# Optimization experiments

Measured on AMD Instinct MI355X. Metric: run time of the kernel, lower is better.

## Reference

```python
import jax, jax.numpy as jnp
import numpy as np

COMMIT_WEIGHT = 0.25


def setup_inputs() -> dict:
    key = jax.random.key(0)
    k1, k2 = jax.random.split(key)
    B, D, T, K = 8, 512, 2048, 8192
    x = jax.random.normal(k1, (B, D, T), dtype=jnp.float32)
    codebook = jax.random.normal(k2, (K, D), dtype=jnp.float32)
    return {"x": x, "codebook": codebook}


def reference(x, codebook):
    # x: [B, D, T] channels-first; VQ operates on [B, T, D]
    xt = jnp.transpose(x, (0, 2, 1))  # [B, T, D]
    x2 = jnp.sum(xt * xt, axis=-1, keepdims=True)          # [B, T, 1]
    e2 = jnp.sum(codebook * codebook, axis=-1)             # [K]
    xe = jnp.einsum('btd,kd->btk', xt, codebook)           # [B, T, K] (dominant GEMM)
    dists = x2 - 2.0 * xe + e2                             # [B, T, K]
    indices = jnp.argmin(dists, axis=-1)                   # [B, T] int
    quantized = codebook[indices]                          # [B, T, D] gather
    # commitment loss: ||sg(q) - x||^2 mean
    commit_loss = COMMIT_WEIGHT * jnp.mean(
        (jax.lax.stop_gradient(quantized) - xt) ** 2)
    # straight-through estimator
    quantized = xt + jax.lax.stop_gradient(quantized - xt)
    quantized = jnp.transpose(quantized, (0, 2, 1))        # back to [B, D, T]
    return quantized, indices, commit_loss
```

## Files before the change

kernel.cpp:

```cpp
#include <hip/hip_runtime.h>
#include <cstdint>
#include <cstddef>

#define B_   8
#define D_   512
#define T_   2048
#define K_   8192
#define BT_  (B_ * T_)
#define NQ_  ((size_t)B_ * D_ * T_)

typedef _Float16 f16x8 __attribute__((ext_vector_type(8)));
typedef _Float16 f16x4 __attribute__((ext_vector_type(4)));
typedef float    f32x4 __attribute__((ext_vector_type(4)));
typedef unsigned long long u64;
typedef unsigned int u32;

#define WS_SLOTS_OFF    0
#define WS_FIDX_OFF     393216
#define WS_PART_OFF     458752
#define WS_E2_OFF       460800
#define WS_XH_OFF       524288
#define WS_XL_OFF       (WS_XH_OFF + 16777216)
#define WS_CH_OFF       (WS_XL_OFF + 16777216)
#define WS_NEEDED       ((size_t)WS_CH_OFF + 8388608)

__device__ __forceinline__ void gload_lds16(const void* g, void* l) {
    __builtin_amdgcn_global_load_lds(
        (const __attribute__((address_space(1))) void*)g,
        (__attribute__((address_space(3))) void*)l, 16, 0, 0);
}

__device__ __forceinline__ u32 fkey(float f) {
    u32 u = __float_as_uint(f);
    u ^= (u32)((int)u >> 31) | 0x80000000u;
    return u;
}
__device__ __forceinline__ u64 umin64(u64 a, u64 b) { return a < b ? a : b; }
__device__ __forceinline__ u64 umax64(u64 a, u64 b) { return a > b ? a : b; }

__global__ __launch_bounds__(256) void k_e2(const float* __restrict__ cb,
                                            float* __restrict__ e2) {
    int k = blockIdx.x * 256 + threadIdx.x;
    const float4* row = (const float4*)(cb + (size_t)k * D_);
    float s = 0.f;
#pragma unroll 4
    for (int i = 0; i < D_ / 4; ++i) {
        float4 v = row[i];
        s = fmaf(v.x, v.x, s); s = fmaf(v.y, v.y, s);
        s = fmaf(v.z, v.z, s); s = fmaf(v.w, v.w, s);
    }
    e2[k] = s;
}

__global__ __launch_bounds__(256) void k_splitcb(const float* __restrict__ cb,
                                                 _Float16* __restrict__ ch) {
    size_t i = ((size_t)blockIdx.x * 256 + threadIdx.x) * 4;
    float4 v = *(const float4*)(cb + i);
    f16x4 h;
    h[0] = (_Float16)v.x; h[1] = (_Float16)v.y;
    h[2] = (_Float16)v.z; h[3] = (_Float16)v.w;
    *(f16x4*)(ch + i) = h;
}

__global__ __launch_bounds__(256) void k_splitx(const float* __restrict__ x,
                                                _Float16* __restrict__ xh,
                                                _Float16* __restrict__ xl) {
    int b  = blockIdx.z;
    int d0 = blockIdx.y * 64;
    int t0 = blockIdx.x * 64;
    int dl = threadIdx.x & 63;
    int tq = threadIdx.x >> 6;
    const float* px = x + ((size_t)b * D_ + (d0 + dl)) * T_ + t0;
#pragma unroll 4
    for (int i = 0; i < 16; ++i) {
        int t = tq * 16 + i;
        float v = px[t];
        _Float16 h = (_Float16)v;
        float lo = v - (float)h;
        _Float16 l = (_Float16)lo;
        size_t row = (size_t)b * T_ + t0 + t;
        xh[row * D_ + d0 + dl] = h;
        xl[row * D_ + d0 + dl] = l;
    }
}

__global__ __launch_bounds__(512, 2)
void k_hi_argmin(const _Float16* __restrict__ xh, const _Float16* __restrict__ ch,
                 const float* __restrict__ e2, u64* __restrict__ slots) {
    __shared__ char smem[131072];
    __shared__ u32 stop[256][2][2];
    __shared__ float e2s[1024];

    const int tid = threadIdx.x;
    const int xcd = blockIdx.x & 7;
    const int bi  = blockIdx.x >> 3;
    const int m_  = bi >> 3;
    const int nblk = bi & 7;
    const int mbase  = (xcd * 8 + m_) * 256;
    const int nstart = nblk * 1024;

    const int lane = tid & 63;
    const int wid  = tid >> 6;
    const int wr = wid & 3, wc = wid >> 2;
    const int lr = lane & 15, lg = lane >> 4;

    {
        u32* p = (u32*)stop;
        p[tid] = ~0u; p[tid + 512] = ~0u;
        *(float2*)&e2s[tid * 2] = *(const float2*)&e2[nstart + tid * 2];
    }
    __syncthreads();

    const bool isA = wid < 4;
    const int q8 = lane >> 3;
    const int u8 = (lane & 7) ^ q8;
    const int srow2 = (u8 >> 2) & 1;
    const int sslot = u8 & 3;
    const char* gs0 = isA
        ? (const char*)xh + (size_t)(mbase  + (wid & 3) * 64 + 2 * q8 + srow2) * 1024
              + sslot * 16
        : (const char*)ch + (size_t)(nstart + (wid & 3) * 64 + 2 * q8 + srow2) * 1024
              + sslot * 16;
    const int ldsbase = (isA ? 0 : 16384) + (wid & 3) * 4096;

#define STAGE2(g, i0) do {                                                   \
        char* lb_ = smem + ((g) & 3) * 32768 + ldsbase;                      \
        const char* gs_ = gs0 + (isA ? 0 : (size_t)((g) >> 4) * 262144)      \
                          + ((g) & 15) * 64;                                 \
        gload_lds16(gs_ + (size_t)(i0) * 16384, lb_ + (i0) * 1024);          \
        gload_lds16(gs_ + (size_t)((i0) + 1) * 16384, lb_ + ((i0) + 1) * 1024); \
    } while (0)

    const int lrh = lr >> 1;
    const int swz16 = ((lg + 4 * (lr & 1)) ^ lrh) * 16;
    const int aoff0 = (wr * 32 + lrh) * 128 + swz16;
    const int boff0 = 16384 + (wc * 64 + lrh) * 128 + swz16;

    u32 top2a[16], top2b[16];
#pragma unroll
    for (int s = 0; s < 16; ++s) { top2a[s] = ~0u; top2b[s] = ~0u; }

    f32x4 acc[4][8];
#pragma unroll
    for (int m = 0; m < 4; ++m)
#pragma unroll
        for (int n = 0; n < 8; ++n)
            acc[m][n] = (f32x4){0.f, 0.f, 0.f, 0.f};

    auto epilogue = [&](int ns) {
        float e2v[8];
#pragma unroll
        for (int n = 0; n < 8; ++n)
            e2v[n] = 0.5f * e2s[ns * 256 + wc * 128 + n * 16 + lr];
        const u32 base10 = ((u32)ns << 8) | ((u32)wc << 7) | (u32)lr;
#pragma unroll
        for (int m = 0; m < 4; ++m) {
#pragma unroll
            for (int j = 0; j < 4; ++j) {
                const int s = m * 4 + j;
                u32 t1 = top2a[s], t2 = top2b[s];
#pragma unroll
                for (int n = 0; n < 8; ++n) {
                    float d = fmaxf(e2v[n] - acc[m][n][j], 1.0f);
                    u32 p = (__float_as_uint(d) & 0xFFFFFC00u) | (base10 + ((u32)n << 4));
                    u32 mx = t1 > p ? t1 : p;
                    t1 = t1 < p ? t1 : p;
                    t2 = t2 < mx ? t2 : mx;
                }
                top2a[s] = t1; top2b[s] = t2;
            }
        }
#pragma unroll
        for (int m = 0; m < 4; ++m)
#pragma unroll
            for (int n = 0; n < 8; ++n)
                acc[m][n] = (f32x4){0.f, 0.f, 0.f, 0.f};
    };

#define MFMA16(AF, BF, NOFF)                                                 \
        __builtin_amdgcn_s_setprio(1);                                       \
        _Pragma("unroll")                                                    \
        for (int m = 0; m < 4; ++m)                                          \
            _Pragma("unroll")                                                \
            for (int n = 0; n < 4; ++n)                                      \
                acc[m][(NOFF) + n] = __builtin_amdgcn_mfma_f32_16x16x32_f16( \
                    AF[m], BF[n], acc[m][(NOFF) + n], 0, 0, 0);              \
        __builtin_amdgcn_s_setprio(0);

#define SB __builtin_amdgcn_sched_barrier(0)

    STAGE2(0, 0); STAGE2(0, 2);
    STAGE2(1, 0); STAGE2(1, 2);
    STAGE2(2, 0); STAGE2(2, 2);
    asm volatile("s_waitcnt vmcnt(8)" ::: "memory");
    __builtin_amdgcn_s_barrier();
    SB;

#pragma unroll 1
    for (int s = 0; s < 64; ++s) {
        const char* base = smem + (s & 3) * 32768;
        f16x8 af[4], bf[4], bg[4];

#pragma unroll
        for (int m = 0; m < 4; ++m)
            af[m] = *(const f16x8*)(base + aoff0 + m * 1024);
#pragma unroll
        for (int n = 0; n < 4; ++n)
            bf[n] = *(const f16x8*)(base + boff0 + n * 1024);
        if (s < 61) STAGE2(s + 3, 0);
        SB;
        MFMA16(af, bf, 0)
        SB;
#pragma unroll
        for (int n = 0; n < 4; ++n)
            bg[n] = *(const f16x8*)(base + boff0 + (4 + n) * 1024);
        if (s < 61) STAGE2(s + 3, 2);
        SB;
        MFMA16(af, bg, 4)
        SB;

        if (s < 61)       asm volatile("s_waitcnt vmcnt(8)" ::: "memory");
        else if (s == 61) asm volatile("s_waitcnt vmcnt(4)" ::: "memory");
        else              asm volatile("s_waitcnt vmcnt(0)" ::: "memory");
        asm volatile("s_waitcnt lgkmcnt(0)" ::: "memory");
        SB;
        __builtin_amdgcn_s_barrier();
        SB;
        if ((s & 15) == 15) epilogue(s >> 4);
    }
#undef STAGE2
#undef MFMA16
#undef SB

#pragma unroll
    for (int m = 0; m < 4; ++m) {
#pragma unroll
        for (int j = 0; j < 4; ++j) {
            const int s = m * 4 + j;
            u32 t1 = top2a[s], t2 = top2b[s];
#pragma unroll
            for (int st = 1; st < 16; st <<= 1) {
                u32 o1 = __shfl_xor(t1, st);
                u32 o2 = __shfl_xor(t2, st);
                u32 mx = t1 > o1 ? t1 : o1;
                u32 sel = t1 < o1 ? t2 : o2;
                u32 n2 = mx < sel ? mx : sel;
                t1 = t1 < o1 ? t1 : o1;
                t2 = t2 < n2 ? t2 : n2;
            }
            if (lr == 0) {
                int ql = wr * 64 + m * 16 + lg * 4 + j;
                stop[ql][wc][0] = t1; stop[ql][wc][1] = t2;
            }
        }
    }

    __syncthreads();
    if (tid < 256) {
        u32 a1 = stop[tid][0][0], a2 = stop[tid][0][1];
        u32 b1 = stop[tid][1][0], b2 = stop[tid][1][1];
        u32 f1 = a1 < b1 ? a1 : b1;
        u32 mx = a1 > b1 ? a1 : b1;
        u32 sel = a1 < b1 ? a2 : b2;
        u32 f2 = mx < sel ? mx : sel;
        int q = mbase + tid;
        u64 p1 = ((u64)(f1 & 0xFFFFFC00u) << 32) | (u32)(nstart + (f1 & 0x3FFu));
        u64 p2 = ((u64)(f2 & 0xFFFFFC00u) << 32) | (u32)(nstart + (f2 & 0x3FFu));
        u64* As = slots + q;
        u64* Bs = slots + BT_ + q;
        u64* Cs = slots + 2 * BT_ + q;
        u64 old = atomicMin(As, p1);
        u64 v = umax64(old, p1);
        old = atomicMin(Bs, v);
        u64 v2 = umax64(old, v);
        atomicMin(Cs, v2);
        old = atomicMin(Bs, p2);
        v = umax64(old, p2);
        atomicMin(Cs, v);
    }
}

__global__ __launch_bounds__(256)
void k_rescore(const _Float16* __restrict__ xh, const _Float16* __restrict__ xl,
               const float* __restrict__ cb, const float* __restrict__ e2,
               const u64* __restrict__ slots,
               u32* __restrict__ final_idx, float* __restrict__ out_idx) {
    const int wid = threadIdx.x >> 6, lane = threadIdx.x & 63;
    const int q = blockIdx.x * 4 + wid;
    u64 a = slots[q], b = slots[BT_ + q], c = slots[2 * BT_ + q];
    u32 i1 = (u32)a, i2 = (u32)b, i3 = (u32)c;
    float d1 = __uint_as_float((u32)(a >> 32));
    float d2 = __uint_as_float((u32)(b >> 32));
    u32 win = i1;
    if (!(d2 - d1 > 0.75f)) {
        float xr[8];
        f16x8 hv = *(const f16x8*)(xh + (size_t)q * D_ + lane * 8);
        f16x8 lv = *(const f16x8*)(xl + (size_t)q * D_ + lane * 8);
#pragma unroll
        for (int i = 0; i < 8; ++i) xr[i] = (float)hv[i] + (float)lv[i];
        u32 idxs[3] = {i1, i2, i3};
        float key[3];
#pragma unroll 1
        for (int cnd = 0; cnd < 3; ++cnd) {
            const float4* cr = (const float4*)(cb + (size_t)idxs[cnd] * D_ + lane * 8);
            float4 c0 = cr[0], c1 = cr[1];
            float s = xr[0] * c0.x;
            s = fmaf(xr[1], c0.y, s); s = fmaf(xr[2], c0.z, s); s = fmaf(xr[3], c0.w, s);
            s = fmaf(xr[4], c1.x, s); s = fmaf(xr[5], c1.y, s);
            s = fmaf(xr[6], c1.z, s); s = fmaf(xr[7], c1.w, s);
#pragma unroll
            for (int st = 1; st < 64; st <<= 1) s += __shfl_xor(s, st);
            key[cnd] = e2[idxs[cnd]] - 2.f * s;
        }
        float bk = key[0]; win = idxs[0];
#pragma unroll
        for (int cnd = 1; cnd < 3; ++cnd) {
            if (key[cnd] < bk || (key[cnd] == bk && idxs[cnd] < win)) {
                bk = key[cnd]; win = idxs[cnd];
            }
        }
    }
    if (lane == 0) { final_idx[q] = win; out_idx[q] = (float)win; }
}

#define MB 64
#define NB 64
#define KC 32
#define FNSPLIT 2
#define KPER (K_ / FNSPLIT)
__global__ __launch_bounds__(256, 2)
void k_argmin_f32(const float* __restrict__ x, const float* __restrict__ cb,
                  const float* __restrict__ e2, u64* __restrict__ slots) {
    __shared__ float xs[KC][MB + 4];
    __shared__ float es[KC][NB + 4];
    __shared__ u64 red[MB];
    const int tid = threadIdx.x;
    const int tx = tid & 15, ty = tid >> 4;
    const int rowtile = blockIdx.x;
    const int b = rowtile >> 5;
    const int tbase = (rowtile & 31) * MB;
    const int nstart = blockIdx.y * KPER;
    if (tid < MB) red[tid] = ~0ull;
    float bestv[4]; int besti[4];
#pragma unroll
    for (int i = 0; i < 4; ++i) { bestv[i] = 3.4e38f; besti[i] = 0; }
    const int sm = tid & 63, sg = tid >> 6;
    const float* xbase = x + (size_t)b * D_ * T_ + (tbase + sm);
    for (int nb = 0; nb < KPER; nb += NB) {
        float acc[4][4];
#pragma unroll
        for (int i = 0; i < 4; ++i)
#pragma unroll
            for (int j = 0; j < 4; ++j) acc[i][j] = 0.f;
        for (int kc = 0; kc < D_; kc += KC) {
            __syncthreads();
#pragma unroll
            for (int r = 0; r < 8; ++r) {
                int dd = sg * 8 + r;
                xs[dd][sm] = xbase[(size_t)(kc + dd) * T_];
            }
            const float* crow = cb + (size_t)(nstart + nb + sm) * D_ + kc + sg * 8;
            float4 c0 = *(const float4*)(crow);
            float4 c1 = *(const float4*)(crow + 4);
            es[sg * 8 + 0][sm] = c0.x; es[sg * 8 + 1][sm] = c0.y;
            es[sg * 8 + 2][sm] = c0.z; es[sg * 8 + 3][sm] = c0.w;
            es[sg * 8 + 4][sm] = c1.x; es[sg * 8 + 5][sm] = c1.y;
            es[sg * 8 + 6][sm] = c1.z; es[sg * 8 + 7][sm] = c1.w;
            __syncthreads();
#pragma unroll
            for (int dd = 0; dd < KC; ++dd) {
                float4 a = *(const float4*)&xs[dd][tx * 4];
                float4 e = *(const float4*)&es[dd][ty * 4];
                acc[0][0] = fmaf(a.x, e.x, acc[0][0]); acc[0][1] = fmaf(a.x, e.y, acc[0][1]);
                acc[0][2] = fmaf(a.x, e.z, acc[0][2]); acc[0][3] = fmaf(a.x, e.w, acc[0][3]);
                acc[1][0] = fmaf(a.y, e.x, acc[1][0]); acc[1][1] = fmaf(a.y, e.y, acc[1][1]);
                acc[1][2] = fmaf(a.y, e.z, acc[1][2]); acc[1][3] = fmaf(a.y, e.w, acc[1][3]);
                acc[2][0] = fmaf(a.z, e.x, acc[2][0]); acc[2][1] = fmaf(a.z, e.y, acc[2][1]);
                acc[2][2] = fmaf(a.z, e.z, acc[2][2]); acc[2][3] = fmaf(a.z, e.w, acc[2][3]);
                acc[3][0] = fmaf(a.w, e.x, acc[3][0]); acc[3][1] = fmaf(a.w, e.y, acc[3][1]);
                acc[3][2] = fmaf(a.w, e.z, acc[3][2]); acc[3][3] = fmaf(a.w, e.w, acc[3][3]);
            }
        }
#pragma unroll
        for (int j = 0; j < 4; ++j) {
            int c = nstart + nb + ty * 4 + j;
            float ec = e2[c];
#pragma unroll
            for (int i = 0; i < 4; ++i) {
                float dist = fmaf(-2.f, acc[i][j], ec);
                if (dist < bestv[i]) { bestv[i] = dist; besti[i] = c; }
            }
        }
    }
    __syncthreads();
#pragma unroll
    for (int i = 0; i < 4; ++i) {
        u64 p = ((u64)fkey(bestv[i]) << 32) | (u32)besti[i];
        atomicMin(&red[tx * 4 + i], p);
    }
    __syncthreads();
    if (tid < MB) atomicMin(&slots[b * T_ + tbase + tid], red[tid]);
}

__global__ __launch_bounds__(256)
void k_finalize(const u64* __restrict__ slots,
                u32* __restrict__ final_idx, float* __restrict__ out_idx) {
    int q = blockIdx.x * 256 + threadIdx.x;
    u32 idx = (u32)slots[q];
    final_idx[q] = idx;
    out_idx[q] = (float)idx;
}

__global__ __launch_bounds__(256)
void k_gather(const float* __restrict__ x, const float* __restrict__ cb,
              const u32* __restrict__ final_idx,
              float* __restrict__ out_q, float* __restrict__ partials) {
    int tid = threadIdx.x;
    int btg = blockIdx.x * 256 + tid;
    int b = btg >> 11, t = btg & (T_ - 1);
    int dch = blockIdx.y;
    u32 idx = final_idx[btg];
    const float* crow = cb + (size_t)idx * D_;
    size_t xoff = (size_t)b * D_ * T_ + t;
    float ls = 0.f;
#pragma unroll 4
    for (int dd = 0; dd < 64; ++dd) {
        int d = dch * 64 + dd;
        float q = crow[d];
        size_t o = xoff + (size_t)d * T_;
        float xv = x[o];
        out_q[o] = q;
        float df = q - xv;
        ls = fmaf(df, df, ls);
    }
    __shared__ float rs[256];
    rs[tid] = ls;
    __syncthreads();
    for (int s = 128; s > 0; s >>= 1) {
        if (tid < s) rs[tid] += rs[tid + s];
        __syncthreads();
    }
    if (tid == 0) partials[blockIdx.y * 64 + blockIdx.x] = rs[0];
}

__global__ __launch_bounds__(256)
void k_loss(const float* __restrict__ partials, float* __restrict__ out_loss) {
    __shared__ float rs[256];
    int tid = threadIdx.x;
    float s = partials[tid] + partials[tid + 256];
    rs[tid] = s;
    __syncthreads();
    for (int st = 128; st > 0; st >>= 1) {
        if (tid < st) rs[tid] += rs[tid + st];
        __syncthreads();
    }
    if (tid == 0) out_loss[0] = 0.25f * rs[0] / (float)NQ_;
}

extern "C" void kernel_launch(void* const* d_in, const int* in_sizes, int n_in,
                              void* d_out, int out_size, void* d_ws, size_t ws_size,
                              hipStream_t stream) {
    const float* x  = (const float*)d_in[0];
    const float* cb = (const float*)d_in[1];

    float* out_q    = (float*)d_out;
    float* out_idx  = out_q + NQ_;
    float* out_loss = out_idx + BT_;

    char* ws = (char*)d_ws;
    u64* slots = (u64*)(ws + WS_SLOTS_OFF);
    u32* fidx = (u32*)(ws + WS_FIDX_OFF);
    float* partials = (float*)(ws + WS_PART_OFF);
    float* e2 = (float*)(ws + WS_E2_OFF);

    hipMemsetAsync(slots, 0xFF, (size_t)3 * BT_ * 8, stream);
    k_e2<<<dim3(K_ / 256), dim3(256), 0, stream>>>(cb, e2);

    if (ws_size >= WS_NEEDED) {
        _Float16* xhp = (_Float16*)(ws + WS_XH_OFF);
        _Float16* xlp = (_Float16*)(ws + WS_XL_OFF);
        _Float16* chp = (_Float16*)(ws + WS_CH_OFF);
        k_splitcb<<<dim3((K_ * D_ / 4) / 256), dim3(256), 0, stream>>>(cb, chp);
        k_splitx<<<dim3(T_ / 64, D_ / 64, B_), dim3(256), 0, stream>>>(x, xhp, xlp);
        k_hi_argmin<<<dim3(512), dim3(512), 0, stream>>>(xhp, chp, e2, slots);
        k_rescore<<<dim3(BT_ / 4), dim3(256), 0, stream>>>(xhp, xlp, cb, e2, slots,
                                                           fidx, out_idx);
    } else {
        k_argmin_f32<<<dim3(BT_ / MB, FNSPLIT), dim3(256), 0, stream>>>(x, cb, e2, slots);
        k_finalize<<<dim3(BT_ / 256), dim3(256), 0, stream>>>(slots, fidx, out_idx);
    }

    k_gather<<<dim3(BT_ / 256, D_ / 64), dim3(256), 0, stream>>>(x, cb, fidx,
                                                                 out_q, partials);
    k_loss<<<dim3(1), dim3(256), 0, stream>>>(partials, out_loss);
}
```

Baseline: 219.8 us.

## Process two K-stages per iteration with full-drain sync and no sched barriers

Restructures the main MFMA loop so each iteration consumes two LDS stages and prefetches the next two stages at the top. Each iteration then ends with a full vmcnt(0) drain before the barrier, replacing the staggered partial waits. The change also removes the s_setprio hints and sched_barrier fences so the compiler can schedule freely. The aim is to halve the barrier count and give loads more time to land. The cost is a shallower rolling pipeline and less control over how instructions interleave.

```diff
diff --git a/kernel.cpp b/kernel.cpp
--- a/kernel.cpp
+++ b/kernel.cpp
@@ -178,59 +178,64 @@
     };
 
 #define MFMA16(AF, BF, NOFF)                                                 \
-        __builtin_amdgcn_s_setprio(1);                                       \
         _Pragma("unroll")                                                    \
         for (int m = 0; m < 4; ++m)                                          \
             _Pragma("unroll")                                                \
             for (int n = 0; n < 4; ++n)                                      \
                 acc[m][(NOFF) + n] = __builtin_amdgcn_mfma_f32_16x16x32_f16( \
-                    AF[m], BF[n], acc[m][(NOFF) + n], 0, 0, 0);              \
-        __builtin_amdgcn_s_setprio(0);
-
-#define SB __builtin_amdgcn_sched_barrier(0)
+                    AF[m], BF[n], acc[m][(NOFF) + n], 0, 0, 0);
 
     STAGE2(0, 0); STAGE2(0, 2);
     STAGE2(1, 0); STAGE2(1, 2);
-    STAGE2(2, 0); STAGE2(2, 2);
-    asm volatile("s_waitcnt vmcnt(8)" ::: "memory");
+    asm volatile("s_waitcnt vmcnt(0)" ::: "memory");
     __builtin_amdgcn_s_barrier();
-    SB;
 
 #pragma unroll 1
-    for (int s = 0; s < 64; ++s) {
-        const char* base = smem + (s & 3) * 32768;
-        f16x8 af[4], bf[4], bg[4];
-
+    for (int p = 0; p < 32; ++p) {
+        const char* baseA = smem + ((2 * p) & 3) * 32768;
+        const char* baseB = smem + ((2 * p + 1) & 3) * 32768;
+
+        if (p < 31) {
+            STAGE2(2 * p + 2, 0); STAGE2(2 * p + 2, 2);
+            STAGE2(2 * p + 3, 0); STAGE2(2 * p + 3, 2);
+        }
+
+        f16x8 af0[4], af1[4], bf[4], bg[4];
 #pragma unroll
         for (int m = 0; m < 4; ++m)
-            af[m] = *(const f16x8*)(base + aoff0 + m * 1024);
+            af0[m] = *(const f16x8*)(baseA + aoff0 + m * 1024);
 #pragma unroll
         for (int n = 0; n < 4; ++n)
-            bf[n] = *(const f16x8*)(base + boff0 + n * 1024);
-        if (s < 61) STAGE2(s + 3, 0);
-        SB;
-        MFMA16(af, bf, 0)
-        SB;
+            bf[n] = *(const f16x8*)(baseA + boff0 + n * 1024);
 #pragma unroll
         for (int n = 0; n < 4; ++n)
-            bg[n] = *(const f16x8*)(base + boff0 + (4 + n) * 1024);
-        if (s < 61) STAGE2(s + 3, 2);
-        SB;
-        MFMA16(af, bg, 4)
-        SB;
-
-        if (s < 61)       asm volatile("s_waitcnt vmcnt(8)" ::: "memory");
-        else if (s == 61) asm volatile("s_waitcnt vmcnt(4)" ::: "memory");
-        else              asm volatile("s_waitcnt vmcnt(0)" ::: "memory");
+            bg[n] = *(const f16x8*)(baseA + boff0 + (4 + n) * 1024);
+#pragma unroll
+        for (int m = 0; m < 4; ++m)
+            af1[m] = *(const f16x8*)(baseB + aoff0 + m * 1024);
+
+        MFMA16(af0, bf, 0)
+
+#pragma unroll
+        for (int n = 0; n < 4; ++n)
+            bf[n] = *(const f16x8*)(baseB + boff0 + n * 1024);
+
+        MFMA16(af0, bg, 4)
+
+#pragma unroll
+        for (int n = 0; n < 4; ++n)
+            bg[n] = *(const f16x8*)(baseB + boff0 + (4 + n) * 1024);
+
+        MFMA16(af1, bf, 0)
+        MFMA16(af1, bg, 4)
+
         asm volatile("s_waitcnt lgkmcnt(0)" ::: "memory");
-        SB;
+        asm volatile("s_waitcnt vmcnt(0)" ::: "memory");
         __builtin_amdgcn_s_barrier();
-        SB;
-        if ((s & 15) == 15) epilogue(s >> 4);
+        if ((p & 7) == 7) epilogue(p >> 3);
     }
 #undef STAGE2
 #undef MFMA16
-#undef SB
 
 #pragma unroll
     for (int m = 0; m < 4; ++m) {
```

Result: faster. 215.1 us (-2.1%).

## Restructure hi-precision argmin GEMM to 4 waves with 128-column N tiles and 3-stage LDS ring

Applied to the files above, without the earlier changes.

The fp16 distance GEMM block drops from 8 waves (4x2 layout, 256x256 tile) to 4 waves that each own 64 rows and share a 128-column codebook tile, so the loop runs twice as many iterations. The LDS pipeline goes from a 4-stage ring of 32KB buffers to a 3-stage ring of 24KB buffers, which frees shared memory for more resident blocks. The cross-wave top-2 merge in LDS is removed because each row is now owned by a single wave. The trade-off is less B-tile reuse per A load, more barriers per unit of work, and a shallower prefetch depth.

```diff
diff --git a/kernel.cpp b/kernel.cpp
--- a/kernel.cpp
+++ b/kernel.cpp
@@ -84,12 +84,12 @@
     }
 }
 
-__global__ __launch_bounds__(512, 2)
+__global__ __launch_bounds__(256, 2)
 void k_hi_argmin(const _Float16* __restrict__ xh, const _Float16* __restrict__ ch,
                  const float* __restrict__ e2, u64* __restrict__ slots) {
-    __shared__ char smem[131072];
-    __shared__ u32 stop[256][2][2];
-    __shared__ float e2s[1024];
+    __shared__ __align__(16) char smem[73728];
+    __shared__ u32 stop[256][2];
+    __shared__ __align__(16) float e2s[1024];
 
     const int tid = threadIdx.x;
     const int xcd = blockIdx.x & 7;
@@ -101,40 +101,35 @@
 
     const int lane = tid & 63;
     const int wid  = tid >> 6;
-    const int wr = wid & 3, wc = wid >> 2;
     const int lr = lane & 15, lg = lane >> 4;
 
     {
         u32* p = (u32*)stop;
-        p[tid] = ~0u; p[tid + 512] = ~0u;
-        *(float2*)&e2s[tid * 2] = *(const float2*)&e2[nstart + tid * 2];
-    }
-    __syncthreads();
-
-    const bool isA = wid < 4;
+        p[tid] = ~0u; p[tid + 256] = ~0u;
+        *(float4*)&e2s[tid * 4] = *(const float4*)&e2[nstart + tid * 4];
+    }
+    __syncthreads();
+
     const int q8 = lane >> 3;
     const int u8 = (lane & 7) ^ q8;
     const int srow2 = (u8 >> 2) & 1;
     const int sslot = u8 & 3;
-    const char* gs0 = isA
-        ? (const char*)xh + (size_t)(mbase  + (wid & 3) * 64 + 2 * q8 + srow2) * 1024
-              + sslot * 16
-        : (const char*)ch + (size_t)(nstart + (wid & 3) * 64 + 2 * q8 + srow2) * 1024
-              + sslot * 16;
-    const int ldsbase = (isA ? 0 : 16384) + (wid & 3) * 4096;
-
-#define STAGE2(g, i0) do {                                                   \
-        char* lb_ = smem + ((g) & 3) * 32768 + ldsbase;                      \
-        const char* gs_ = gs0 + (isA ? 0 : (size_t)((g) >> 4) * 262144)      \
-                          + ((g) & 15) * 64;                                 \
-        gload_lds16(gs_ + (size_t)(i0) * 16384, lb_ + (i0) * 1024);          \
-        gload_lds16(gs_ + (size_t)((i0) + 1) * 16384, lb_ + ((i0) + 1) * 1024); \
-    } while (0)
+    const char* gsA = (const char*)xh
+        + (size_t)(mbase + wid * 64 + 2 * q8 + srow2) * 1024 + sslot * 16;
+    const char* gsB = (const char*)ch
+        + (size_t)(nstart + wid * 32 + 2 * q8 + srow2) * 1024 + sslot * 16;
+
+#define STA(slot, g, i) gload_lds16(                                         \
+        gsA + (size_t)(i) * 16384 + ((g) & 15) * 64,                         \
+        smem + (slot) * 24576 + wid * 4096 + (i) * 1024 + lane * 16)
+#define STB(slot, g, i) gload_lds16(                                         \
+        gsB + (size_t)((g) >> 4) * 131072 + (size_t)(i) * 16384 + ((g) & 15) * 64, \
+        smem + (slot) * 24576 + 16384 + wid * 2048 + (i) * 1024 + lane * 16)
 
     const int lrh = lr >> 1;
     const int swz16 = ((lg + 4 * (lr & 1)) ^ lrh) * 16;
-    const int aoff0 = (wr * 32 + lrh) * 128 + swz16;
-    const int boff0 = 16384 + (wc * 64 + lrh) * 128 + swz16;
+    const int aoff0 = wid * 4096 + lrh * 128 + swz16;
+    const int boff0 = 16384 + lrh * 128 + swz16;
 
     u32 top2a[16], top2b[16];
 #pragma unroll
@@ -151,8 +146,8 @@
         float e2v[8];
 #pragma unroll
         for (int n = 0; n < 8; ++n)
-            e2v[n] = 0.5f * e2s[ns * 256 + wc * 128 + n * 16 + lr];
-        const u32 base10 = ((u32)ns << 8) | ((u32)wc << 7) | (u32)lr;
+            e2v[n] = 0.5f * e2s[ns * 128 + n * 16 + lr];
+        const u32 base10 = ((u32)ns << 7) | (u32)lr;
 #pragma unroll
         for (int m = 0; m < 4; ++m) {
 #pragma unroll
@@ -189,16 +184,17 @@
 
 #define SB __builtin_amdgcn_sched_barrier(0)
 
-    STAGE2(0, 0); STAGE2(0, 2);
-    STAGE2(1, 0); STAGE2(1, 2);
-    STAGE2(2, 0); STAGE2(2, 2);
-    asm volatile("s_waitcnt vmcnt(8)" ::: "memory");
+    STA(0, 0, 0); STA(0, 0, 1); STA(0, 0, 2); STA(0, 0, 3); STB(0, 0, 0); STB(0, 0, 1);
+    STA(1, 1, 0); STA(1, 1, 1); STA(1, 1, 2); STA(1, 1, 3); STB(1, 1, 0); STB(1, 1, 1);
+    asm volatile("s_waitcnt vmcnt(6)" ::: "memory");
     __builtin_amdgcn_s_barrier();
     SB;
 
+    int cs = 0;
 #pragma unroll 1
-    for (int s = 0; s < 64; ++s) {
-        const char* base = smem + (s & 3) * 32768;
+    for (int s = 0; s < 128; ++s) {
+        const char* base = smem + cs * 24576;
+        const int ps = (cs == 0) ? 2 : cs - 1;
         f16x8 af[4], bf[4], bg[4];
 
 #pragma unroll
@@ -207,28 +203,29 @@
 #pragma unroll
         for (int n = 0; n < 4; ++n)
             bf[n] = *(const f16x8*)(base + boff0 + n * 1024);
-        if (s < 61) STAGE2(s + 3, 0);
+        if (s < 126) { STA(ps, s + 2, 0); STA(ps, s + 2, 1); STB(ps, s + 2, 0); }
         SB;
         MFMA16(af, bf, 0)
         SB;
 #pragma unroll
         for (int n = 0; n < 4; ++n)
             bg[n] = *(const f16x8*)(base + boff0 + (4 + n) * 1024);
-        if (s < 61) STAGE2(s + 3, 2);
+        if (s < 126) { STA(ps, s + 2, 2); STA(ps, s + 2, 3); STB(ps, s + 2, 1); }
         SB;
         MFMA16(af, bg, 4)
         SB;
 
-        if (s < 61)       asm volatile("s_waitcnt vmcnt(8)" ::: "memory");
-        else if (s == 61) asm volatile("s_waitcnt vmcnt(4)" ::: "memory");
-        else              asm volatile("s_waitcnt vmcnt(0)" ::: "memory");
+        if (s < 126) asm volatile("s_waitcnt vmcnt(6)" ::: "memory");
+        else         asm volatile("s_waitcnt vmcnt(0)" ::: "memory");
         asm volatile("s_waitcnt lgkmcnt(0)" ::: "memory");
         SB;
         __builtin_amdgcn_s_barrier();
         SB;
+        cs = (cs == 2) ? 0 : cs + 1;
         if ((s & 15) == 15) epilogue(s >> 4);
     }
-#undef STAGE2
+#undef STA
+#undef STB
 #undef MFMA16
 #undef SB
 
@@ -249,20 +246,15 @@
                 t2 = t2 < n2 ? t2 : n2;
             }
             if (lr == 0) {
-                int ql = wr * 64 + m * 16 + lg * 4 + j;
-                stop[ql][wc][0] = t1; stop[ql][wc][1] = t2;
-            }
-        }
-    }
-
-    __syncthreads();
-    if (tid < 256) {
-        u32 a1 = stop[tid][0][0], a2 = stop[tid][0][1];
-        u32 b1 = stop[tid][1][0], b2 = stop[tid][1][1];
-        u32 f1 = a1 < b1 ? a1 : b1;
-        u32 mx = a1 > b1 ? a1 : b1;
-        u32 sel = a1 < b1 ? a2 : b2;
-        u32 f2 = mx < sel ? mx : sel;
+                int ql = wid * 64 + m * 16 + lg * 4 + j;
+                stop[ql][0] = t1; stop[ql][1] = t2;
+            }
+        }
+    }
+
+    __syncthreads();
+    {
+        u32 f1 = stop[tid][0], f2 = stop[tid][1];
         int q = mbase + tid;
         u64 p1 = ((u64)(f1 & 0xFFFFFC00u) << 32) | (u32)(nstart + (f1 & 0x3FFu));
         u64 p2 = ((u64)(f2 & 0xFFFFFC00u) << 32) | (u32)(nstart + (f2 & 0x3FFu));
@@ -482,7 +474,7 @@
         _Float16* chp = (_Float16*)(ws + WS_CH_OFF);
         k_splitcb<<<dim3((K_ * D_ / 4) / 256), dim3(256), 0, stream>>>(cb, chp);
         k_splitx<<<dim3(T_ / 64, D_ / 64, B_), dim3(256), 0, stream>>>(x, xhp, xlp);
-        k_hi_argmin<<<dim3(512), dim3(512), 0, stream>>>(xhp, chp, e2, slots);
+        k_hi_argmin<<<dim3(512), dim3(256), 0, stream>>>(xhp, chp, e2, slots);
         k_rescore<<<dim3(BT_ / 4), dim3(256), 0, stream>>>(xhp, xlp, cb, e2, slots,
                                                            fidx, out_idx);
     } else {
```

After: 222.9 us. No clear change (+1.4%).
